# Kernel tuning notes

Measured on AMD Instinct MI355X. Metric: run time of the kernel, lower is better.

The kernel has to match this reference:

```python
import jax, jax.numpy as jnp
import numpy as np

B, L, H, NH = 8, 200, 128, 4
DH = H // NH
NEG = -2.0**32 + 1.0


def setup_inputs() -> dict:
    key = jax.random.key(0)
    ks = jax.random.split(key, 14)
    f = lambda k, s, sc=1.0: jax.random.normal(k, s, dtype=jnp.float32) * sc
    inp = {
        "queries": f(ks[0], (B, L, H)),
        "keys": f(ks[1], (B, L, H)),
        "time_mask": jax.random.bernoulli(ks[2], 0.1, (B, L)),  # True = padded query row
        "attn_mask": jnp.triu(jnp.ones((L, L), dtype=bool), k=1),  # True = masked (causal)
        "time_matrix_K": f(ks[3], (B, L, L, H), 0.5),
        "time_matrix_V": f(ks[4], (B, L, L, H), 0.5),
        "abs_pos_K": f(ks[5], (B, L, H), 0.5),
        "abs_pos_V": f(ks[6], (B, L, H), 0.5),
        "Qw": f(ks[7], (H, H), H ** -0.5),
        "Qb": f(ks[8], (H,), 0.02),
        "Kw": f(ks[9], (H, H), H ** -0.5),
        "Kb": f(ks[10], (H,), 0.02),
        "Vw": f(ks[11], (H, H), H ** -0.5),
        "Vb": f(ks[12], (H,), 0.02),
    }
    return inp


def reference(queries, keys, time_mask, attn_mask, time_matrix_K, time_matrix_V,
              abs_pos_K, abs_pos_V, Qw, Qb, Kw, Kb, Vw, Vb):
    # Linear projections (torch Linear: x @ W.T + b)
    Q = queries @ Qw.T + Qb                      # [B,L,H]
    K = keys @ Kw.T + Kb
    V = keys @ Vw.T + Vb
    # head split: torch cat(split(.., head_size, dim=-1), dim=0) == contiguous head chunks
    Qh = Q.reshape(B, L, NH, DH)
    Kh = K.reshape(B, L, NH, DH)
    Vh = V.reshape(B, L, NH, DH)
    pKh = abs_pos_K.reshape(B, L, NH, DH)
    pVh = abs_pos_V.reshape(B, L, NH, DH)
    tKh = time_matrix_K.reshape(B, L, L, NH, DH)
    tVh = time_matrix_V.reshape(B, L, L, NH, DH)

    # attention logits: content + absolute-position bias + relative-time bias
    attn = jnp.einsum('blhd,bmhd->bhlm', Qh, Kh)
    attn += jnp.einsum('blhd,bmhd->bhlm', Qh, pKh)
    attn += jnp.einsum('blmhd,blhd->bhlm', tKh, Qh)
    attn = attn / (DH ** 0.5)

    mask = time_mask[:, None, :, None] | attn_mask[None, None, :, :]  # [B,1,L,L] -> broadcast
    attn = jnp.where(mask, NEG, attn)
    attn = jax.nn.softmax(attn, axis=-1)         # [B,NH,L,L]

    out = jnp.einsum('bhlm,bmhd->blhd', attn, Vh)
    out += jnp.einsum('bhlm,bmhd->blhd', attn, pVh)
    out += jnp.einsum('bhlm,blmhd->blhd', attn, tVh)
    return out.reshape(B, L, H)
```

## Files before the change

### kernel.cpp

```cpp
#include <hip/hip_runtime.h>
#include <math.h>

#define B 8
#define L 200
#define H 128
#define NH 4
#define DH 32
#define NEGV (-4294967295.0f)

__global__ __launch_bounds__(128) void proj_kernel(
    const float* __restrict__ queries, const float* __restrict__ keys,
    const float* __restrict__ apK, const float* __restrict__ apV,
    const float* __restrict__ Qw, const float* __restrict__ Qb,
    const float* __restrict__ Kw, const float* __restrict__ Kb,
    const float* __restrict__ Vw, const float* __restrict__ Vb,
    float* __restrict__ Qo, float* __restrict__ Kpo, float* __restrict__ Vpo)
{
    const int j    = threadIdx.x;
    const int row0 = blockIdx.x * 8;

    __shared__ float4 qrow[8 * 32];
    __shared__ float4 krow[8 * 32];

    const float4* q4 = (const float4*)queries + row0 * 32;
    const float4* k4 = (const float4*)keys    + row0 * 32;
    for (int idx = j; idx < 256; idx += 128) { qrow[idx] = q4[idx]; krow[idx] = k4[idx]; }
    __syncthreads();

    float accQ[8], accK[8], accV[8];
    const float qb = Qb[j], kb = Kb[j], vb = Vb[j];
    #pragma unroll
    for (int r = 0; r < 8; ++r) { accQ[r] = qb; accK[r] = kb; accV[r] = vb; }

    const float4* Qw4 = (const float4*)Qw + j * 32;
    const float4* Kw4 = (const float4*)Kw + j * 32;
    const float4* Vw4 = (const float4*)Vw + j * 32;

    for (int k = 0; k < 32; ++k) {
        const float4 wq = Qw4[k];
        const float4 wk = Kw4[k];
        const float4 wv = Vw4[k];
        #pragma unroll
        for (int r = 0; r < 8; ++r) {
            const float4 x = qrow[r * 32 + k];
            accQ[r] = fmaf(wq.x, x.x, fmaf(wq.y, x.y, fmaf(wq.z, x.z, fmaf(wq.w, x.w, accQ[r]))));
            const float4 y = krow[r * 32 + k];
            accK[r] = fmaf(wk.x, y.x, fmaf(wk.y, y.y, fmaf(wk.z, y.z, fmaf(wk.w, y.w, accK[r]))));
            accV[r] = fmaf(wv.x, y.x, fmaf(wv.y, y.y, fmaf(wv.z, y.z, fmaf(wv.w, y.w, accV[r]))));
        }
    }

    #pragma unroll
    for (int r = 0; r < 8; ++r) {
        const int i = row0 + r;
        Qo [i * H + j] = accQ[r];
        Kpo[i * H + j] = accK[r] + apK[i * H + j];
        Vpo[i * H + j] = accV[r] + apV[i * H + j];
    }
}

__global__ __launch_bounds__(512) void attn_kernel(
    const float* __restrict__ Qo, const float* __restrict__ Kp,
    const float* __restrict__ Vp,
    const float* __restrict__ tK, const float* __restrict__ tV,
    const int* __restrict__ tmask, float* __restrict__ out)
{
    const int bl = blockIdx.x;
    const int b  = bl / L;
    const int l  = bl % L;
    const int t  = threadIdx.x;
    const int c4   = t & 31;
    const int part = t >> 5;
    const int h    = c4 >> 3;

    __shared__ float  S[NH * L];
    __shared__ float4 P[32 * 17];

    const bool rowmasked = (tmask[bl] != 0);
    const float4 q = ((const float4*)Qo)[bl * 32 + c4];

    const float4* Kp4 = (const float4*)Kp + (size_t)b * L * 32;
    const float4* tK4 = (const float4*)tK + (size_t)bl * L * 32;

    #pragma unroll
    for (int i = 0; i < 3; ++i) {
        float4 kk[4], tt[4];
        #pragma unroll
        for (int u = 0; u < 4; ++u) {
            const int m = part + 16 * (4 * i + u);
            kk[u] = Kp4[m * 32 + c4];
            tt[u] = tK4[m * 32 + c4];
        }
        #pragma unroll
        for (int u = 0; u < 4; ++u) {
            const int m = part + 16 * (4 * i + u);
            float v = fmaf(q.x, kk[u].x + tt[u].x,
                      fmaf(q.y, kk[u].y + tt[u].y,
                      fmaf(q.z, kk[u].z + tt[u].z,
                           q.w * (kk[u].w + tt[u].w))));
            v += __shfl_down(v, 4, 8);
            v += __shfl_down(v, 2, 8);
            v += __shfl_down(v, 1, 8);
            if ((t & 7) == 0) {
                const bool masked = rowmasked || (m > l);
                S[h * L + m] = masked ? NEGV : v * 0.17677669529663687f;
            }
        }
    }
    if (part < 8) {
        const int m = part + 192;
        const float4 kk = Kp4[m * 32 + c4];
        const float4 tt = tK4[m * 32 + c4];
        float v = fmaf(q.x, kk.x + tt.x,
                  fmaf(q.y, kk.y + tt.y,
                  fmaf(q.z, kk.z + tt.z,
                       q.w * (kk.w + tt.w))));
        v += __shfl_down(v, 4, 8);
        v += __shfl_down(v, 2, 8);
        v += __shfl_down(v, 1, 8);
        if ((t & 7) == 0) {
            const bool masked = rowmasked || (m > l);
            S[h * L + m] = masked ? NEGV : v * 0.17677669529663687f;
        }
    }
    __syncthreads();

    if (t < 256) {
        const int hw   = t >> 6;
        const int lane = t & 63;
        float mx = -INFINITY;
        for (int m = lane; m < L; m += 64) mx = fmaxf(mx, S[hw * L + m]);
        #pragma unroll
        for (int off = 32; off; off >>= 1) mx = fmaxf(mx, __shfl_xor(mx, off));
        float s = 0.0f;
        for (int m = lane; m < L; m += 64) s += __expf(S[hw * L + m] - mx);
        #pragma unroll
        for (int off = 32; off; off >>= 1) s += __shfl_xor(s, off);
        const float inv = 1.0f / s;
        for (int m = lane; m < L; m += 64)
            S[hw * L + m] = __expf(S[hw * L + m] - mx) * inv;
    }
    __syncthreads();

    const float4* Vp4 = (const float4*)Vp + (size_t)b * L * 32;
    const float4* tV4 = (const float4*)tV + (size_t)bl * L * 32;
    float4 acc = make_float4(0.f, 0.f, 0.f, 0.f);
    #pragma unroll
    for (int i = 0; i < 3; ++i) {
        float4 vv[4], tt[4];
        #pragma unroll
        for (int u = 0; u < 4; ++u) {
            const int m = part + 16 * (4 * i + u);
            vv[u] = Vp4[m * 32 + c4];
            tt[u] = tV4[m * 32 + c4];
        }
        #pragma unroll
        for (int u = 0; u < 4; ++u) {
            const int m = part + 16 * (4 * i + u);
            const float w = S[h * L + m];
            acc.x = fmaf(w, vv[u].x + tt[u].x, acc.x);
            acc.y = fmaf(w, vv[u].y + tt[u].y, acc.y);
            acc.z = fmaf(w, vv[u].z + tt[u].z, acc.z);
            acc.w = fmaf(w, vv[u].w + tt[u].w, acc.w);
        }
    }
    if (part < 8) {
        const int m = part + 192;
        const float w = S[h * L + m];
        const float4 vv = Vp4[m * 32 + c4];
        const float4 tt = tV4[m * 32 + c4];
        acc.x = fmaf(w, vv.x + tt.x, acc.x);
        acc.y = fmaf(w, vv.y + tt.y, acc.y);
        acc.z = fmaf(w, vv.z + tt.z, acc.z);
        acc.w = fmaf(w, vv.w + tt.w, acc.w);
    }
    P[c4 * 17 + part] = acc;
    __syncthreads();

    if (t < 32) {
        float4 tot = make_float4(0.f, 0.f, 0.f, 0.f);
        #pragma unroll
        for (int p = 0; p < 16; ++p) {
            const float4 a = P[t * 17 + p];
            tot.x += a.x; tot.y += a.y; tot.z += a.z; tot.w += a.w;
        }
        ((float4*)out)[bl * 32 + t] = tot;
    }
}

extern "C" void kernel_launch(void* const* d_in, const int* in_sizes, int n_in,
                              void* d_out, int out_size, void* d_ws, size_t ws_size,
                              hipStream_t stream) {
    const float* queries = (const float*)d_in[0];
    const float* keys    = (const float*)d_in[1];
    const int*   tmask   = (const int*)d_in[2];
    const float* tK   = (const float*)d_in[4];
    const float* tV   = (const float*)d_in[5];
    const float* apK  = (const float*)d_in[6];
    const float* apV  = (const float*)d_in[7];
    const float* Qw   = (const float*)d_in[8];
    const float* Qb   = (const float*)d_in[9];
    const float* Kw   = (const float*)d_in[10];
    const float* Kb   = (const float*)d_in[11];
    const float* Vw   = (const float*)d_in[12];
    const float* Vb   = (const float*)d_in[13];
    float* out = (float*)d_out;

    float* Qo  = (float*)d_ws;
    float* Kpo = Qo  + (size_t)B * L * H;
    float* Vpo = Kpo + (size_t)B * L * H;

    proj_kernel<<<(B * L) / 8, 128, 0, stream>>>(
        queries, keys, apK, apV, Qw, Qb, Kw, Kb, Vw, Vb, Qo, Kpo, Vpo);

    attn_kernel<<<B * L, 512, 0, stream>>>(Qo, Kpo, Vpo, tK, tV, tmask, out);
}
```

Measured before the change: 377.9 us.

## Skip causally masked keys and reverse block order for load balance

The attention kernel now loads and processes only keys m <= l for each query row. This skips the masked half of the time_matrix_K/V reads, roughly half of the memory traffic. Fully padded rows skip the QK stage and softmax and use uniform weights 1/L over all keys, which matches softmax over equal NEG values. Blocks are remapped so the longest rows (large l) launch first, with batch interleaved, to balance the now uneven per-block work. The loops become dynamic with predicated loads, so the compiler loses full unrolling.

Result: faster. 344.2 us (-8.9%).

```diff
diff --git a/kernel.cpp b/kernel.cpp
--- a/kernel.cpp
+++ b/kernel.cpp
@@ -65,9 +65,10 @@
     const float* __restrict__ tK, const float* __restrict__ tV,
     const int* __restrict__ tmask, float* __restrict__ out)
 {
-    const int bl = blockIdx.x;
-    const int b  = bl / L;
-    const int l  = bl % L;
+    const int bid = blockIdx.x;
+    const int b   = bid & 7;
+    const int l   = 199 - (bid >> 3);
+    const int bl  = b * L + l;
     const int t  = threadIdx.x;
     const int c4   = t & 31;
     const int part = t >> 5;
@@ -82,97 +83,86 @@
     const float4* Kp4 = (const float4*)Kp + (size_t)b * L * 32;
     const float4* tK4 = (const float4*)tK + (size_t)bl * L * 32;
 
-    #pragma unroll
-    for (int i = 0; i < 3; ++i) {
-        float4 kk[4], tt[4];
-        #pragma unroll
-        for (int u = 0; u < 4; ++u) {
-            const int m = part + 16 * (4 * i + u);
-            kk[u] = Kp4[m * 32 + c4];
-            tt[u] = tK4[m * 32 + c4];
-        }
-        #pragma unroll
-        for (int u = 0; u < 4; ++u) {
-            const int m = part + 16 * (4 * i + u);
-            float v = fmaf(q.x, kk[u].x + tt[u].x,
-                      fmaf(q.y, kk[u].y + tt[u].y,
-                      fmaf(q.z, kk[u].z + tt[u].z,
-                           q.w * (kk[u].w + tt[u].w))));
-            v += __shfl_down(v, 4, 8);
-            v += __shfl_down(v, 2, 8);
-            v += __shfl_down(v, 1, 8);
-            if ((t & 7) == 0) {
-                const bool masked = rowmasked || (m > l);
-                S[h * L + m] = masked ? NEGV : v * 0.17677669529663687f;
-            }
-        }
-    }
-    if (part < 8) {
-        const int m = part + 192;
-        const float4 kk = Kp4[m * 32 + c4];
-        const float4 tt = tK4[m * 32 + c4];
-        float v = fmaf(q.x, kk.x + tt.x,
-                  fmaf(q.y, kk.y + tt.y,
-                  fmaf(q.z, kk.z + tt.z,
-                       q.w * (kk.w + tt.w))));
-        v += __shfl_down(v, 4, 8);
-        v += __shfl_down(v, 2, 8);
-        v += __shfl_down(v, 1, 8);
-        if ((t & 7) == 0) {
-            const bool masked = rowmasked || (m > l);
-            S[h * L + m] = masked ? NEGV : v * 0.17677669529663687f;
-        }
-    }
-    __syncthreads();
-
-    if (t < 256) {
+    if (!rowmasked) {
+        const int nsteps = (l + 16) >> 4;
+        for (int i0 = 0; i0 < nsteps; i0 += 4) {
+            float4 kk[4], tt[4];
+            int mm[4];
+            #pragma unroll
+            for (int u = 0; u < 4; ++u) {
+                const int m = part + 16 * (i0 + u);
+                mm[u] = m;
+                if (m <= l) {
+                    kk[u] = Kp4[m * 32 + c4];
+                    tt[u] = tK4[m * 32 + c4];
+                }
+            }
+            #pragma unroll
+            for (int u = 0; u < 4; ++u) {
+                const int m = mm[u];
+                float v = 0.0f;
+                if (m <= l) {
+                    v = fmaf(q.x, kk[u].x + tt[u].x,
+                        fmaf(q.y, kk[u].y + tt[u].y,
+                        fmaf(q.z, kk[u].z + tt[u].z,
+                             q.w * (kk[u].w + tt[u].w))));
+                }
+                v += __shfl_down(v, 4, 8);
+                v += __shfl_down(v, 2, 8);
+                v += __shfl_down(v, 1, 8);
+                if ((t & 7) == 0 && m <= l)
+                    S[h * L + m] = v * 0.17677669529663687f;
+            }
+        }
+    }
+    __syncthreads();
+
+    if (!rowmasked && t < 256) {
         const int hw   = t >> 6;
         const int lane = t & 63;
         float mx = -INFINITY;
-        for (int m = lane; m < L; m += 64) mx = fmaxf(mx, S[hw * L + m]);
+        for (int m = lane; m <= l; m += 64) mx = fmaxf(mx, S[hw * L + m]);
         #pragma unroll
         for (int off = 32; off; off >>= 1) mx = fmaxf(mx, __shfl_xor(mx, off));
         float s = 0.0f;
-        for (int m = lane; m < L; m += 64) s += __expf(S[hw * L + m] - mx);
+        for (int m = lane; m <= l; m += 64) s += __expf(S[hw * L + m] - mx);
         #pragma unroll
         for (int off = 32; off; off >>= 1) s += __shfl_xor(s, off);
         const float inv = 1.0f / s;
-        for (int m = lane; m < L; m += 64)
+        for (int m = lane; m <= l; m += 64)
             S[hw * L + m] = __expf(S[hw * L + m] - mx) * inv;
     }
     __syncthreads();
 
     const float4* Vp4 = (const float4*)Vp + (size_t)b * L * 32;
     const float4* tV4 = (const float4*)tV + (size_t)bl * L * 32;
+    const int   nmV = rowmasked ? L : (l + 1);
+    const float wU  = 1.0f / (float)L;
     float4 acc = make_float4(0.f, 0.f, 0.f, 0.f);
-    #pragma unroll
-    for (int i = 0; i < 3; ++i) {
+    const int nstepsV = (nmV + 15) >> 4;
+    for (int i0 = 0; i0 < nstepsV; i0 += 4) {
         float4 vv[4], tt[4];
+        int mm[4];
         #pragma unroll
         for (int u = 0; u < 4; ++u) {
-            const int m = part + 16 * (4 * i + u);
-            vv[u] = Vp4[m * 32 + c4];
-            tt[u] = tV4[m * 32 + c4];
+            const int m = part + 16 * (i0 + u);
+            mm[u] = m;
+            if (m < nmV) {
+                vv[u] = Vp4[m * 32 + c4];
+                tt[u] = tV4[m * 32 + c4];
+            }
         }
         #pragma unroll
         for (int u = 0; u < 4; ++u) {
-            const int m = part + 16 * (4 * i + u);
-            const float w = S[h * L + m];
-            acc.x = fmaf(w, vv[u].x + tt[u].x, acc.x);
-            acc.y = fmaf(w, vv[u].y + tt[u].y, acc.y);
-            acc.z = fmaf(w, vv[u].z + tt[u].z, acc.z);
-            acc.w = fmaf(w, vv[u].w + tt[u].w, acc.w);
-        }
-    }
-    if (part < 8) {
-        const int m = part + 192;
-        const float w = S[h * L + m];
-        const float4 vv = Vp4[m * 32 + c4];
-        const float4 tt = tV4[m * 32 + c4];
-        acc.x = fmaf(w, vv.x + tt.x, acc.x);
-        acc.y = fmaf(w, vv.y + tt.y, acc.y);
-        acc.z = fmaf(w, vv.z + tt.z, acc.z);
-        acc.w = fmaf(w, vv.w + tt.w, acc.w);
+            const int m = mm[u];
+            if (m < nmV) {
+                const float w = rowmasked ? wU : S[h * L + m];
+                acc.x = fmaf(w, vv[u].x + tt[u].x, acc.x);
+                acc.y = fmaf(w, vv[u].y + tt[u].y, acc.y);
+                acc.z = fmaf(w, vv[u].z + tt[u].z, acc.z);
+                acc.w = fmaf(w, vv[u].w + tt[u].w, acc.w);
+            }
+        }
     }
     P[c4 * 17 + part] = acc;
     __syncthreads();
```
